# Kernel tuning notes

Hardware: AMD Instinct MI355X
Metric: run time of the kernel (lower is better)

## Reference

```python
import jax, jax.numpy as jnp
import numpy as np

B, A, H, V, L = 8192, 128, 256, 64, 20


def setup_inputs() -> dict:
    key = jax.random.key(0)
    ks = jax.random.split(key, 9)
    s = lambda k, sh: jax.random.normal(k, sh, dtype=jnp.float32) * 0.05
    return {
        "attrVector": jax.random.normal(ks[0], (B, A), dtype=jnp.float32),
        "W_a": s(ks[1], (H, A)), "b_a": s(ks[2], (H,)),
        "W_ih": s(ks[3], (4 * H, V)), "W_hh": s(ks[4], (4 * H, H)),
        "b_ih": s(ks[5], (4 * H,)), "b_hh": s(ks[6], (4 * H,)),
        "W_v": s(ks[7], (V, H)), "b_v": s(ks[8], (V,)),
    }


def _lstm_step(x, h, c, W_ih, W_hh, b_ih, b_hh):
    # PyTorch LSTM gate order: input, forget, cell(g), output
    gates = x @ W_ih.T + b_ih + h @ W_hh.T + b_hh  # [B, 4H]
    i, f, g, o = jnp.split(gates, 4, axis=-1)
    c_new = jax.nn.sigmoid(f) * c + jax.nn.sigmoid(i) * jnp.tanh(g)
    h_new = jax.nn.sigmoid(o) * jnp.tanh(c_new)
    return h_new, c_new


def reference(attrVector, W_a, b_a, W_ih, W_hh, b_ih, b_hh, W_v, b_v):
    batch = attrVector.shape[0]
    dt = attrVector.dtype
    # attr2hidden -> initial hidden state; cell state zeros (init_hidden)
    h = attrVector @ W_a.T + b_a                      # [B, H]
    c = jnp.zeros_like(h)
    # start-token step (all-zeros embedding)
    x0 = jnp.zeros((batch, V), dtype=dt)
    h, c = _lstm_step(x0, h, c, W_ih, W_hh, b_ih, b_hh)

    keys = jax.random.split(jax.random.key(42), L)

    def step(carry, k):
        h, c, slp, plp, ep = carry
        logits = h @ W_v.T + b_v                      # [B, V]
        logp = jax.nn.log_softmax(logits, axis=-1)
        plp = plp + jnp.sum(jnp.exp(logp) * logp, axis=-1)  # negative entropy
        ch = jax.random.categorical(k, logits, axis=-1)     # [B] int sample
        lp = jnp.take_along_axis(logp, ch[:, None], axis=-1)[:, 0]
        slp = slp + lp
        ep = ep * jnp.exp(lp)
        x = jax.nn.one_hot(ch, V, dtype=dt)
        h2, c2 = _lstm_step(x, h, c, W_ih, W_hh, b_ih, b_hh)
        return (h2, c2, slp, plp, ep), ch

    zeros = jnp.zeros((batch,), dtype=dt)
    ones = jnp.ones((batch,), dtype=dt)
    (_, _, slp, plp, ep), msgs = jax.lax.scan(step, (h, c, zeros, zeros, ones), keys)
    message = msgs.T.astype(jnp.int64) if msgs.dtype != jnp.int64 else msgs.T  # [B, L]
    return message, slp, plp, ep
```

## Files before the change

### kernel.cpp

```cpp
#include <hip/hip_runtime.h>
#include <stdint.h>

#define BATCH 8192
#define ADIM 128
#define HDIM 256
#define VDIM 64
#define NSTEP 20
#define TB 16
#define HSP 17
#define ASP 20

typedef union { float4 v; float f[4]; } F4;

__device__ __forceinline__ uint32_t rotl32(uint32_t x, uint32_t d) {
  return (x << d) | (x >> (32u - d));
}
__device__ __forceinline__ void tf4(uint32_t& x0, uint32_t& x1, int r0, int r1, int r2, int r3) {
  x0 += x1; x1 = rotl32(x1, r0); x1 ^= x0;
  x0 += x1; x1 = rotl32(x1, r1); x1 ^= x0;
  x0 += x1; x1 = rotl32(x1, r2); x1 ^= x0;
  x0 += x1; x1 = rotl32(x1, r3); x1 ^= x0;
}
__device__ __forceinline__ void threefry2x32(uint32_t k0, uint32_t k1, uint32_t x0, uint32_t x1,
                                             uint32_t& o0, uint32_t& o1) {
  uint32_t k2 = k0 ^ k1 ^ 0x1BD11BDAu;
  x0 += k0; x1 += k1;
  tf4(x0, x1, 13, 15, 26, 6);  x0 += k1; x1 += k2 + 1u;
  tf4(x0, x1, 17, 29, 16, 24); x0 += k2; x1 += k0 + 2u;
  tf4(x0, x1, 13, 15, 26, 6);  x0 += k0; x1 += k1 + 3u;
  tf4(x0, x1, 17, 29, 16, 24); x0 += k1; x1 += k2 + 4u;
  tf4(x0, x1, 13, 15, 26, 6);  x0 += k2; x1 += k0 + 5u;
  o0 = x0; o1 = x1;
}

__device__ __forceinline__ float sigm(float x) { return 1.0f / (1.0f + expf(-x)); }

__device__ __forceinline__ float bcast(float x, int t) {
  return __int_as_float(__builtin_amdgcn_readlane(__float_as_int(x), t));
}

__global__ void prep_kernel(const float* __restrict__ Whh, const float* __restrict__ Wv,
                            const float* __restrict__ Wa, const float* __restrict__ Wih,
                            float* __restrict__ ws) {
  int n = blockIdx.x * blockDim.x + threadIdx.x;
  int stride = gridDim.x * blockDim.x;
  float* WhhT4 = ws;
  float* WvT   = ws + 262144;
  float* WaT   = ws + 278528;
  float* WihT4 = ws + 311296;
  for (int i = n; i < 256 * 1024; i += stride) {
    int k = i >> 10, rem = i & 1023, u = rem >> 2, g = rem & 3;
    WhhT4[i] = Whh[((g << 8) + u) * 256 + k];
  }
  for (int i = n; i < 256 * 64; i += stride) { int k = i >> 6, v = i & 63; WvT[i] = Wv[v * 256 + k]; }
  for (int i = n; i < 128 * 256; i += stride) { int k = i >> 8, u = i & 255; WaT[i] = Wa[u * 128 + k]; }
  for (int i = n; i < 64 * 1024; i += stride) {
    int v = i >> 10, rem = i & 1023, u = rem >> 2, g = rem & 3;
    WihT4[i] = Wih[((g << 8) + u) * 64 + v];
  }
}

__global__ __launch_bounds__(256, 2) void sender_main(
    const float* __restrict__ attr, const float* __restrict__ b_a,
    const float* __restrict__ b_ih, const float* __restrict__ b_hh,
    const float* __restrict__ b_v,
    const float* __restrict__ WhhT4, const float* __restrict__ WvT,
    const float* __restrict__ WaT, const float* __restrict__ WihT4,
    float* __restrict__ out) {
  __shared__ float h_s[HDIM][HSP];
  __shared__ __align__(16) float attr_s[ADIM][ASP];
  __shared__ float slp_s[TB], plp_s[TB], ep_s[TB];
  __shared__ int ch_s[TB];

  const int tid = threadIdx.x;
  const int w = tid >> 6;
  const int lane = tid & 63;
  const int u = (w << 6) + lane;
  const int w4 = w << 2;
  const int b0 = blockIdx.x * TB;

  if (tid < TB) { slp_s[tid] = 0.0f; plp_s[tid] = 0.0f; ep_s[tid] = 1.0f; }

  {
    int r = tid >> 5;
    int cm = (tid & 31) << 2;
    #pragma unroll
    for (int pass = 0; pass < 2; ++pass) {
      int row = r + (pass << 3);
      F4 vv; vv.v = *(const float4*)&attr[(size_t)(b0 + row) * ADIM + cm];
      attr_s[cm + 0][row] = vv.f[0];
      attr_s[cm + 1][row] = vv.f[1];
      attr_s[cm + 2][row] = vv.f[2];
      attr_s[cm + 3][row] = vv.f[3];
    }
  }
  __syncthreads();

  {
    float acc[16];
    #pragma unroll
    for (int s = 0; s < 16; ++s) acc[s] = 0.0f;
    #pragma unroll 2
    for (int k = 0; k < ADIM; ++k) {
      F4 a0, a1, a2, a3;
      a0.v = *(const float4*)&attr_s[k][0];
      a1.v = *(const float4*)&attr_s[k][4];
      a2.v = *(const float4*)&attr_s[k][8];
      a3.v = *(const float4*)&attr_s[k][12];
      float wa = WaT[(k << 8) + u];
      #pragma unroll
      for (int j = 0; j < 4; ++j) {
        acc[j]      = fmaf(a0.f[j], wa, acc[j]);
        acc[4 + j]  = fmaf(a1.f[j], wa, acc[4 + j]);
        acc[8 + j]  = fmaf(a2.f[j], wa, acc[8 + j]);
        acc[12 + j] = fmaf(a3.f[j], wa, acc[12 + j]);
      }
    }
    float ba = b_a[u];
    #pragma unroll
    for (int s = 0; s < 16; ++s) h_s[u][s] = acc[s] + ba;
  }
  __syncthreads();

  float c_r[16];
  #pragma unroll
  for (int s = 0; s < 16; ++s) c_r[s] = 0.0f;

  float bg[4];
  #pragma unroll
  for (int g = 0; g < 4; ++g) bg[g] = b_ih[(g << 8) + u] + b_hh[(g << 8) + u];
  const float bv = b_v[lane];

  {
    float ga[16][4];
    #pragma unroll
    for (int s = 0; s < 16; ++s)
      #pragma unroll
      for (int g = 0; g < 4; ++g) ga[s][g] = 0.0f;
    #pragma unroll 1
    for (int kc = 0; kc < 16; ++kc) {
      const int k0 = kc << 4;
      const int kk = k0 + (lane & 15);
      float hch[16];
      #pragma unroll
      for (int s = 0; s < 16; ++s) hch[s] = h_s[kk][(s + w4) & 15];
      #pragma unroll
      for (int t = 0; t < 16; ++t) {
        const int k = k0 + t;
        F4 wv4; wv4.v = *(const float4*)&WhhT4[(k << 10) + (u << 2)];
        #pragma unroll
        for (int s = 0; s < 16; ++s) {
          float hb = bcast(hch[s], t);
          ga[s][0] = fmaf(hb, wv4.f[0], ga[s][0]);
          ga[s][1] = fmaf(hb, wv4.f[1], ga[s][1]);
          ga[s][2] = fmaf(hb, wv4.f[2], ga[s][2]);
          ga[s][3] = fmaf(hb, wv4.f[3], ga[s][3]);
        }
      }
    }
    __syncthreads();
    float hn[16];
    #pragma unroll
    for (int s = 0; s < 16; ++s) {
      float gi = ga[s][0] + bg[0];
      float gf = ga[s][1] + bg[1];
      float gg = ga[s][2] + bg[2];
      float go = ga[s][3] + bg[3];
      float cn = sigm(gf) * c_r[s] + sigm(gi) * tanhf(gg);
      hn[s] = sigm(go) * tanhf(cn);
      c_r[s] = cn;
    }
    #pragma unroll
    for (int s = 0; s < 16; ++s) h_s[u][(s + w4) & 15] = hn[s];
    __syncthreads();
  }

  #pragma unroll 1
  for (int l = 0; l < NSTEP; ++l) {
    uint32_t kl0, kl1;
    threefry2x32(0u, 42u, 0u, (uint32_t)l, kl0, kl1);

    const bool last = (l == NSTEP - 1);
    float la[4] = {0.0f, 0.0f, 0.0f, 0.0f};
    float ga[16][4];
    #pragma unroll
    for (int s = 0; s < 16; ++s)
      #pragma unroll
      for (int g = 0; g < 4; ++g) ga[s][g] = 0.0f;

    if (!last) {
      #pragma unroll 1
      for (int kc = 0; kc < 16; ++kc) {
        const int k0 = kc << 4;
        const int kk = k0 + (lane & 15);
        float hch[16];
        #pragma unroll
        for (int s = 0; s < 16; ++s) hch[s] = h_s[kk][(s + w4) & 15];
        #pragma unroll
        for (int t = 0; t < 16; ++t) {
          const int k = k0 + t;
          F4 wv4; wv4.v = *(const float4*)&WhhT4[(k << 10) + (u << 2)];
          float wvv = WvT[(k << 6) | lane];
          #pragma unroll
          for (int s = 0; s < 16; ++s) {
            float hb = bcast(hch[s], t);
            if (s < 4) la[s] = fmaf(hb, wvv, la[s]);
            ga[s][0] = fmaf(hb, wv4.f[0], ga[s][0]);
            ga[s][1] = fmaf(hb, wv4.f[1], ga[s][1]);
            ga[s][2] = fmaf(hb, wv4.f[2], ga[s][2]);
            ga[s][3] = fmaf(hb, wv4.f[3], ga[s][3]);
          }
        }
      }
    } else {
      #pragma unroll 1
      for (int kc = 0; kc < 16; ++kc) {
        const int k0 = kc << 4;
        const int kk = k0 + (lane & 15);
        float hch[4];
        #pragma unroll
        for (int s = 0; s < 4; ++s) hch[s] = h_s[kk][(s + w4) & 15];
        #pragma unroll
        for (int t = 0; t < 16; ++t) {
          const int k = k0 + t;
          float wvv = WvT[(k << 6) | lane];
          #pragma unroll
          for (int s = 0; s < 4; ++s) la[s] = fmaf(bcast(hch[s], t), wvv, la[s]);
        }
      }
    }

    #pragma unroll
    for (int db = 0; db < 4; ++db) {
      float x = la[db] + bv;
      float m = x;
      #pragma unroll
      for (int o = 32; o > 0; o >>= 1) m = fmaxf(m, __shfl_xor(m, o));
      float e = expf(x - m);
      float s = e;
      #pragma unroll
      for (int o = 32; o > 0; o >>= 1) s += __shfl_xor(s, o);
      float lse = logf(s);
      float logp = x - m - lse;
      float p = expf(logp);
      float pe = p * logp;
      #pragma unroll
      for (int o = 32; o > 0; o >>= 1) pe += __shfl_xor(pe, o);
      uint32_t idx = ((uint32_t)(b0 + w4 + db) << 6) | (uint32_t)lane;
      uint32_t r0, r1;
      threefry2x32(kl0, kl1, 0u, idx, r0, r1);
      uint32_t bits = r0 ^ r1;
      float f01 = __uint_as_float((bits >> 9) | 0x3f800000u) - 1.0f;
      const float TINY = 1.17549435e-38f;
      float uu2 = fmaxf(TINY, f01 + TINY);
      float gn = -logf(-logf(uu2));
      float y = gn + x;
      float by = y; int bi = lane;
      #pragma unroll
      for (int o = 32; o > 0; o >>= 1) {
        float oy = __shfl_xor(by, o);
        int oi = __shfl_xor(bi, o);
        if (oy > by || (oy == by && oi < bi)) { by = oy; bi = oi; }
      }
      float lp = __shfl(logp, bi, 64);
      if (lane == 0) {
        int bb = w4 + db;
        ch_s[bb] = bi;
        slp_s[bb] += lp;
        plp_s[bb] += pe;
        ep_s[bb] *= expf(lp);
        out[(size_t)(b0 + bb) * NSTEP + l] = (float)bi;
      }
    }

    if (!last) {
      __syncthreads();
      float hn[16];
      #pragma unroll
      for (int s = 0; s < 16; ++s) {
        const int sp = (s + w4) & 15;
        F4 wi; wi.v = *(const float4*)&WihT4[(ch_s[sp] << 10) + (u << 2)];
        float gi = ga[s][0] + wi.f[0] + bg[0];
        float gf = ga[s][1] + wi.f[1] + bg[1];
        float gg = ga[s][2] + wi.f[2] + bg[2];
        float go = ga[s][3] + wi.f[3] + bg[3];
        float cn = sigm(gf) * c_r[s] + sigm(gi) * tanhf(gg);
        hn[s] = sigm(go) * tanhf(cn);
        c_r[s] = cn;
      }
      #pragma unroll
      for (int s = 0; s < 16; ++s) h_s[u][(s + w4) & 15] = hn[s];
      __syncthreads();
    }
  }

  __syncthreads();
  if (tid < TB) {
    int bb = b0 + tid;
    out[(size_t)BATCH * NSTEP + bb]             = slp_s[tid];
    out[(size_t)BATCH * NSTEP + BATCH + bb]     = plp_s[tid];
    out[(size_t)BATCH * NSTEP + 2 * BATCH + bb] = ep_s[tid];
  }
}

extern "C" void kernel_launch(void* const* d_in, const int* in_sizes, int n_in,
                              void* d_out, int out_size, void* d_ws, size_t ws_size,
                              hipStream_t stream) {
  const float* attr = (const float*)d_in[0];
  const float* W_a  = (const float*)d_in[1];
  const float* b_a  = (const float*)d_in[2];
  const float* W_ih = (const float*)d_in[3];
  const float* W_hh = (const float*)d_in[4];
  const float* b_ih = (const float*)d_in[5];
  const float* b_hh = (const float*)d_in[6];
  const float* W_v  = (const float*)d_in[7];
  const float* b_v  = (const float*)d_in[8];
  float* ws = (float*)d_ws;

  prep_kernel<<<256, 256, 0, stream>>>(W_hh, W_v, W_a, W_ih, ws);
  sender_main<<<BATCH / TB, 256, 0, stream>>>(
      attr, b_a, b_ih, b_hh, b_v,
      ws, ws + 262144, ws + 278528, ws + 311296,
      (float*)d_out);
}
```

Baseline: 1.451 ms.

## Store hidden state batch-major and read it with broadcast float4 LDS loads

Changes the shared hidden-state layout from [H][17] to [TB][H]. Each wave now reads four consecutive hidden values per sample with a uniform-address float4 LDS load, replacing the per-k readlane broadcasts. The vocab projection reads W_v directly in its row layout with float4 loads, so the WvT transpose in the prep kernel is dropped. This cuts readlane instructions and scalar dependencies but moves more traffic onto LDS reads, and the hidden-state stores now have a different bank pattern.

```diff
diff --git a/kernel.cpp b/kernel.cpp
--- a/kernel.cpp
+++ b/kernel.cpp
@@ -7,7 +7,6 @@
 #define VDIM 64
 #define NSTEP 20
 #define TB 16
-#define HSP 17
 #define ASP 20
 
 typedef union { float4 v; float f[4]; } F4;
@@ -35,28 +34,21 @@
 
 __device__ __forceinline__ float sigm(float x) { return 1.0f / (1.0f + expf(-x)); }
 
-__device__ __forceinline__ float bcast(float x, int t) {
-  return __int_as_float(__builtin_amdgcn_readlane(__float_as_int(x), t));
-}
-
-__global__ void prep_kernel(const float* __restrict__ Whh, const float* __restrict__ Wv,
-                            const float* __restrict__ Wa, const float* __restrict__ Wih,
-                            float* __restrict__ ws) {
+__global__ void prep_kernel(const float* __restrict__ Whh, const float* __restrict__ Wa,
+                            const float* __restrict__ Wih, float* __restrict__ ws) {
   int n = blockIdx.x * blockDim.x + threadIdx.x;
   int stride = gridDim.x * blockDim.x;
   float* WhhT4 = ws;
-  float* WvT   = ws + 262144;
-  float* WaT   = ws + 278528;
-  float* WihT4 = ws + 311296;
+  float* WaT   = ws + 262144;
+  float* WihT4 = ws + 294912;
   for (int i = n; i < 256 * 1024; i += stride) {
     int k = i >> 10, rem = i & 1023, u = rem >> 2, g = rem & 3;
     WhhT4[i] = Whh[((g << 8) + u) * 256 + k];
   }
-  for (int i = n; i < 256 * 64; i += stride) { int k = i >> 6, v = i & 63; WvT[i] = Wv[v * 256 + k]; }
-  for (int i = n; i < 128 * 256; i += stride) { int k = i >> 8, u = i & 255; WaT[i] = Wa[u * 128 + k]; }
+  for (int i = n; i < 128 * 256; i += stride) { int k = i >> 8, uu = i & 255; WaT[i] = Wa[uu * 128 + k]; }
   for (int i = n; i < 64 * 1024; i += stride) {
-    int v = i >> 10, rem = i & 1023, u = rem >> 2, g = rem & 3;
-    WihT4[i] = Wih[((g << 8) + u) * 64 + v];
+    int v = i >> 10, rem = i & 1023, uu = rem >> 2, g = rem & 3;
+    WihT4[i] = Wih[((g << 8) + uu) * 64 + v];
   }
 }
 
@@ -64,10 +56,10 @@
     const float* __restrict__ attr, const float* __restrict__ b_a,
     const float* __restrict__ b_ih, const float* __restrict__ b_hh,
     const float* __restrict__ b_v,
-    const float* __restrict__ WhhT4, const float* __restrict__ WvT,
+    const float* __restrict__ WhhT4, const float* __restrict__ Wv2,
     const float* __restrict__ WaT, const float* __restrict__ WihT4,
     float* __restrict__ out) {
-  __shared__ float h_s[HDIM][HSP];
+  __shared__ __align__(16) float h_s[TB][HDIM];
   __shared__ __align__(16) float attr_s[ADIM][ASP];
   __shared__ float slp_s[TB], plp_s[TB], ep_s[TB];
   __shared__ int ch_s[TB];
@@ -76,8 +68,15 @@
   const int w = tid >> 6;
   const int lane = tid & 63;
   const int u = (w << 6) + lane;
+  const int uu4 = u << 2;
   const int w4 = w << 2;
   const int b0 = blockIdx.x * TB;
+
+  int hr[16];
+  #pragma unroll
+  for (int s = 0; s < 16; ++s) hr[s] = (s + w4) & 15;
+
+  const float* Wv2r = Wv2 + (lane << 8);
 
   if (tid < TB) { slp_s[tid] = 0.0f; plp_s[tid] = 0.0f; ep_s[tid] = 1.0f; }
 
@@ -118,7 +117,7 @@
     }
     float ba = b_a[u];
     #pragma unroll
-    for (int s = 0; s < 16; ++s) h_s[u][s] = acc[s] + ba;
+    for (int s = 0; s < 16; ++s) h_s[s][u] = acc[s] + ba;
   }
   __syncthreads();
 
@@ -139,22 +138,24 @@
       for (int g = 0; g < 4; ++g) ga[s][g] = 0.0f;
     #pragma unroll 1
     for (int kc = 0; kc < 16; ++kc) {
-      const int k0 = kc << 4;
-      const int kk = k0 + (lane & 15);
-      float hch[16];
-      #pragma unroll
-      for (int s = 0; s < 16; ++s) hch[s] = h_s[kk][(s + w4) & 15];
-      #pragma unroll
-      for (int t = 0; t < 16; ++t) {
-        const int k = k0 + t;
-        F4 wv4; wv4.v = *(const float4*)&WhhT4[(k << 10) + (u << 2)];
+      #pragma unroll
+      for (int kg = 0; kg < 4; ++kg) {
+        const int k0 = (kc << 4) + (kg << 2);
+        F4 wk[4];
+        #pragma unroll
+        for (int j = 0; j < 4; ++j)
+          wk[j].v = *(const float4*)&WhhT4[((k0 + j) << 10) + uu4];
         #pragma unroll
         for (int s = 0; s < 16; ++s) {
-          float hb = bcast(hch[s], t);
-          ga[s][0] = fmaf(hb, wv4.f[0], ga[s][0]);
-          ga[s][1] = fmaf(hb, wv4.f[1], ga[s][1]);
-          ga[s][2] = fmaf(hb, wv4.f[2], ga[s][2]);
-          ga[s][3] = fmaf(hb, wv4.f[3], ga[s][3]);
+          F4 h4; h4.v = *(const float4*)&h_s[hr[s]][k0];
+          #pragma unroll
+          for (int j = 0; j < 4; ++j) {
+            float hb = h4.f[j];
+            ga[s][0] = fmaf(hb, wk[j].f[0], ga[s][0]);
+            ga[s][1] = fmaf(hb, wk[j].f[1], ga[s][1]);
+            ga[s][2] = fmaf(hb, wk[j].f[2], ga[s][2]);
+            ga[s][3] = fmaf(hb, wk[j].f[3], ga[s][3]);
+          }
         }
       }
     }
@@ -171,7 +172,7 @@
       c_r[s] = cn;
     }
     #pragma unroll
-    for (int s = 0; s < 16; ++s) h_s[u][(s + w4) & 15] = hn[s];
+    for (int s = 0; s < 16; ++s) h_s[hr[s]][u] = hn[s];
     __syncthreads();
   }
 
@@ -191,41 +192,49 @@
     if (!last) {
       #pragma unroll 1
       for (int kc = 0; kc < 16; ++kc) {
-        const int k0 = kc << 4;
-        const int kk = k0 + (lane & 15);
-        float hch[16];
         #pragma unroll
-        for (int s = 0; s < 16; ++s) hch[s] = h_s[kk][(s + w4) & 15];
-        #pragma unroll
-        for (int t = 0; t < 16; ++t) {
-          const int k = k0 + t;
-          F4 wv4; wv4.v = *(const float4*)&WhhT4[(k << 10) + (u << 2)];
-          float wvv = WvT[(k << 6) | lane];
+        for (int kg = 0; kg < 4; ++kg) {
+          const int k0 = (kc << 4) + (kg << 2);
+          F4 wk[4], wvv;
+          #pragma unroll
+          for (int j = 0; j < 4; ++j)
+            wk[j].v = *(const float4*)&WhhT4[((k0 + j) << 10) + uu4];
+          wvv.v = *(const float4*)(Wv2r + k0);
           #pragma unroll
           for (int s = 0; s < 16; ++s) {
-            float hb = bcast(hch[s], t);
-            if (s < 4) la[s] = fmaf(hb, wvv, la[s]);
-            ga[s][0] = fmaf(hb, wv4.f[0], ga[s][0]);
-            ga[s][1] = fmaf(hb, wv4.f[1], ga[s][1]);
-            ga[s][2] = fmaf(hb, wv4.f[2], ga[s][2]);
-            ga[s][3] = fmaf(hb, wv4.f[3], ga[s][3]);
+            F4 h4; h4.v = *(const float4*)&h_s[hr[s]][k0];
+            if (s < 4) {
+              la[s] = fmaf(h4.f[0], wvv.f[0], la[s]);
+              la[s] = fmaf(h4.f[1], wvv.f[1], la[s]);
+              la[s] = fmaf(h4.f[2], wvv.f[2], la[s]);
+              la[s] = fmaf(h4.f[3], wvv.f[3], la[s]);
+            }
+            #pragma unroll
+            for (int j = 0; j < 4; ++j) {
+              float hb = h4.f[j];
+              ga[s][0] = fmaf(hb, wk[j].f[0], ga[s][0]);
+              ga[s][1] = fmaf(hb, wk[j].f[1], ga[s][1]);
+              ga[s][2] = fmaf(hb, wk[j].f[2], ga[s][2]);
+              ga[s][3] = fmaf(hb, wk[j].f[3], ga[s][3]);
+            }
           }
         }
       }
     } else {
       #pragma unroll 1
       for (int kc = 0; kc < 16; ++kc) {
-        const int k0 = kc << 4;
-        const int kk = k0 + (lane & 15);
-        float hch[4];
         #pragma unroll
-        for (int s = 0; s < 4; ++s) hch[s] = h_s[kk][(s + w4) & 15];
-        #pragma unroll
-        for (int t = 0; t < 16; ++t) {
-          const int k = k0 + t;
-          float wvv = WvT[(k << 6) | lane];
+        for (int kg = 0; kg < 4; ++kg) {
+          const int k0 = (kc << 4) + (kg << 2);
+          F4 wvv; wvv.v = *(const float4*)(Wv2r + k0);
           #pragma unroll
-          for (int s = 0; s < 4; ++s) la[s] = fmaf(bcast(hch[s], t), wvv, la[s]);
+          for (int s = 0; s < 4; ++s) {
+            F4 h4; h4.v = *(const float4*)&h_s[hr[s]][k0];
+            la[s] = fmaf(h4.f[0], wvv.f[0], la[s]);
+            la[s] = fmaf(h4.f[1], wvv.f[1], la[s]);
+            la[s] = fmaf(h4.f[2], wvv.f[2], la[s]);
+            la[s] = fmaf(h4.f[3], wvv.f[3], la[s]);
+          }
         }
       }
     }
@@ -278,8 +287,8 @@
       float hn[16];
       #pragma unroll
       for (int s = 0; s < 16; ++s) {
-        const int sp = (s + w4) & 15;
-        F4 wi; wi.v = *(const float4*)&WihT4[(ch_s[sp] << 10) + (u << 2)];
+        const int sp = hr[s];
+        F4 wi; wi.v = *(const float4*)&WihT4[(ch_s[sp] << 10) + uu4];
         float gi = ga[s][0] + wi.f[0] + bg[0];
         float gf = ga[s][1] + wi.f[1] + bg[1];
         float gg = ga[s][2] + wi.f[2] + bg[2];
@@ -289,7 +298,7 @@
         c_r[s] = cn;
       }
       #pragma unroll
-      for (int s = 0; s < 16; ++s) h_s[u][(s + w4) & 15] = hn[s];
+      for (int s = 0; s < 16; ++s) h_s[hr[s]][u] = hn[s];
       __syncthreads();
     }
   }
@@ -317,9 +326,9 @@
   const float* b_v  = (const float*)d_in[8];
   float* ws = (float*)d_ws;
 
-  prep_kernel<<<256, 256, 0, stream>>>(W_hh, W_v, W_a, W_ih, ws);
+  prep_kernel<<<256, 256, 0, stream>>>(W_hh, W_a, W_ih, ws);
   sender_main<<<BATCH / TB, 256, 0, stream>>>(
       attr, b_a, b_ih, b_hh, b_v,
-      ws, ws + 262144, ws + 278528, ws + 311296,
+      ws, W_v, ws + 262144, ws + 294912,
       (float*)d_out);
 }
```

After: 1.876 ms. 29.3% more time.

## Use packed FP32 FMA inline asm and move cell state to LDS

Applied to the files above, without the earlier changes.

Replaces the scalar FMA inner loop of the recurrent GEMV with hand-written inline asm. It reads two h values per lane pair into SGPRs and applies v_pk_fma_f32 over gate pairs, which halves the FMA instruction count. The cell state moves from registers into shared memory to free VGPRs for the 2-waves-per-SIMD launch bound. The cost is extra LDS traffic and fixed SGPR clobbers that can limit compiler scheduling. The h_s write also moves inside the same loop, without the earlier staging array.

```diff
diff --git a/kernel.cpp b/kernel.cpp
--- a/kernel.cpp
+++ b/kernel.cpp
@@ -10,7 +10,8 @@
 #define HSP 17
 #define ASP 20
 
-typedef union { float4 v; float f[4]; } F4;
+typedef float v2f __attribute__((ext_vector_type(2)));
+typedef union { float4 v; v2f h2[2]; float f[4]; } F4;
 
 __device__ __forceinline__ uint32_t rotl32(uint32_t x, uint32_t d) {
   return (x << d) | (x >> (32u - d));
@@ -53,12 +54,72 @@
     WhhT4[i] = Whh[((g << 8) + u) * 256 + k];
   }
   for (int i = n; i < 256 * 64; i += stride) { int k = i >> 6, v = i & 63; WvT[i] = Wv[v * 256 + k]; }
-  for (int i = n; i < 128 * 256; i += stride) { int k = i >> 8, u = i & 255; WaT[i] = Wa[u * 128 + k]; }
+  for (int i = n; i < 128 * 256; i += stride) { int k = i >> 8, uu = i & 255; WaT[i] = Wa[uu * 128 + k]; }
   for (int i = n; i < 64 * 1024; i += stride) {
-    int v = i >> 10, rem = i & 1023, u = rem >> 2, g = rem & 3;
-    WihT4[i] = Wih[((g << 8) + u) * 64 + v];
-  }
-}
+    int v = i >> 10, rem = i & 1023, uu = rem >> 2, g = rem & 3;
+    WihT4[i] = Wih[((g << 8) + uu) * 64 + v];
+  }
+}
+
+#define SPBLK(SA, SB, T0, T1)                                                              \
+  asm("v_readlane_b32 s90, %[ha], " #T0 "\n\t"                                             \
+      "v_readlane_b32 s91, %[ha], " #T1 "\n\t"                                             \
+      "v_readlane_b32 s92, %[hb], " #T0 "\n\t"                                             \
+      "v_readlane_b32 s93, %[hb], " #T1 "\n\t"                                             \
+      "v_pk_fma_f32 %[aA0], s[90:91], %[w0A], %[aA0] op_sel:[0,0,0] op_sel_hi:[0,1,1]\n\t" \
+      "v_pk_fma_f32 %[aA1], s[90:91], %[w1A], %[aA1] op_sel:[0,0,0] op_sel_hi:[0,1,1]\n\t" \
+      "v_pk_fma_f32 %[aA0], s[90:91], %[w0B], %[aA0] op_sel:[1,0,0] op_sel_hi:[1,1,1]\n\t" \
+      "v_pk_fma_f32 %[aA1], s[90:91], %[w1B], %[aA1] op_sel:[1,0,0] op_sel_hi:[1,1,1]\n\t" \
+      "v_pk_fma_f32 %[aB0], s[92:93], %[w0A], %[aB0] op_sel:[0,0,0] op_sel_hi:[0,1,1]\n\t" \
+      "v_pk_fma_f32 %[aB1], s[92:93], %[w1A], %[aB1] op_sel:[0,0,0] op_sel_hi:[0,1,1]\n\t" \
+      "v_pk_fma_f32 %[aB0], s[92:93], %[w0B], %[aB0] op_sel:[1,0,0] op_sel_hi:[1,1,1]\n\t" \
+      "v_pk_fma_f32 %[aB1], s[92:93], %[w1B], %[aB1] op_sel:[1,0,0] op_sel_hi:[1,1,1]"     \
+      : [aA0]"+v"(ga01[SA]), [aA1]"+v"(ga23[SA]),                                          \
+        [aB0]"+v"(ga01[SB]), [aB1]"+v"(ga23[SB])                                           \
+      : [ha]"v"(hch[SA]), [hb]"v"(hch[SB]),                                                \
+        [w0A]"v"(wkA.h2[0]), [w1A]"v"(wkA.h2[1]),                                          \
+        [w0B]"v"(wkB.h2[0]), [w1B]"v"(wkB.h2[1])                                           \
+      : "s90","s91","s92","s93")
+
+#define SPBLK_L(SA, SB, T0, T1)                                                            \
+  asm("v_readlane_b32 s90, %[ha], " #T0 "\n\t"                                             \
+      "v_readlane_b32 s91, %[ha], " #T1 "\n\t"                                             \
+      "v_readlane_b32 s92, %[hb], " #T0 "\n\t"                                             \
+      "v_readlane_b32 s93, %[hb], " #T1 "\n\t"                                             \
+      "v_pk_fma_f32 %[aA0], s[90:91], %[w0A], %[aA0] op_sel:[0,0,0] op_sel_hi:[0,1,1]\n\t" \
+      "v_pk_fma_f32 %[aA1], s[90:91], %[w1A], %[aA1] op_sel:[0,0,0] op_sel_hi:[0,1,1]\n\t" \
+      "v_pk_fma_f32 %[aA0], s[90:91], %[w0B], %[aA0] op_sel:[1,0,0] op_sel_hi:[1,1,1]\n\t" \
+      "v_pk_fma_f32 %[aA1], s[90:91], %[w1B], %[aA1] op_sel:[1,0,0] op_sel_hi:[1,1,1]\n\t" \
+      "v_fma_f32 %[lA], s90, %[wv0], %[lA]\n\t"                                            \
+      "v_fma_f32 %[lA], s91, %[wv1], %[lA]\n\t"                                            \
+      "v_pk_fma_f32 %[aB0], s[92:93], %[w0A], %[aB0] op_sel:[0,0,0] op_sel_hi:[0,1,1]\n\t" \
+      "v_pk_fma_f32 %[aB1], s[92:93], %[w1A], %[aB1] op_sel:[0,0,0] op_sel_hi:[0,1,1]\n\t" \
+      "v_pk_fma_f32 %[aB0], s[92:93], %[w0B], %[aB0] op_sel:[1,0,0] op_sel_hi:[1,1,1]\n\t" \
+      "v_pk_fma_f32 %[aB1], s[92:93], %[w1B], %[aB1] op_sel:[1,0,0] op_sel_hi:[1,1,1]\n\t" \
+      "v_fma_f32 %[lB], s92, %[wv0], %[lB]\n\t"                                            \
+      "v_fma_f32 %[lB], s93, %[wv1], %[lB]"                                                \
+      : [aA0]"+v"(ga01[SA]), [aA1]"+v"(ga23[SA]),                                          \
+        [aB0]"+v"(ga01[SB]), [aB1]"+v"(ga23[SB]),                                          \
+        [lA]"+v"(la[SA]), [lB]"+v"(la[SB])                                                 \
+      : [ha]"v"(hch[SA]), [hb]"v"(hch[SB]),                                                \
+        [w0A]"v"(wkA.h2[0]), [w1A]"v"(wkA.h2[1]),                                          \
+        [w0B]"v"(wkB.h2[0]), [w1B]"v"(wkB.h2[1]),                                          \
+        [wv0]"v"(wv0), [wv1]"v"(wv1)                                                       \
+      : "s90","s91","s92","s93")
+
+#define TPAIR(T0, T1)                                                  \
+  do {                                                                 \
+    F4 wkA, wkB;                                                       \
+    wkA.v = *(const float4*)&WhhT4[((k0 + T0) << 10) + uu4];           \
+    wkB.v = *(const float4*)&WhhT4[((k0 + T1) << 10) + uu4];           \
+    float wv0 = WvT[((k0 + T0) << 6) | lane];                          \
+    float wv1 = WvT[((k0 + T1) << 6) | lane];                          \
+    SPBLK_L(0, 1, T0, T1);                                             \
+    SPBLK_L(2, 3, T0, T1);                                             \
+    SPBLK(4, 5, T0, T1);   SPBLK(6, 7, T0, T1);                        \
+    SPBLK(8, 9, T0, T1);   SPBLK(10, 11, T0, T1);                      \
+    SPBLK(12, 13, T0, T1); SPBLK(14, 15, T0, T1);                      \
+  } while (0)
 
 __global__ __launch_bounds__(256, 2) void sender_main(
     const float* __restrict__ attr, const float* __restrict__ b_a,
@@ -68,6 +129,7 @@
     const float* __restrict__ WaT, const float* __restrict__ WihT4,
     float* __restrict__ out) {
   __shared__ float h_s[HDIM][HSP];
+  __shared__ float c_s[HDIM][HSP];
   __shared__ __align__(16) float attr_s[ADIM][ASP];
   __shared__ float slp_s[TB], plp_s[TB], ep_s[TB];
   __shared__ int ch_s[TB];
@@ -76,6 +138,7 @@
   const int w = tid >> 6;
   const int lane = tid & 63;
   const int u = (w << 6) + lane;
+  const int uu4 = u << 2;
   const int w4 = w << 2;
   const int b0 = blockIdx.x * TB;
 
@@ -122,10 +185,6 @@
   }
   __syncthreads();
 
-  float c_r[16];
-  #pragma unroll
-  for (int s = 0; s < 16; ++s) c_r[s] = 0.0f;
-
   float bg[4];
   #pragma unroll
   for (int g = 0; g < 4; ++g) bg[g] = b_ih[(g << 8) + u] + b_hh[(g << 8) + u];
@@ -147,7 +206,7 @@
       #pragma unroll
       for (int t = 0; t < 16; ++t) {
         const int k = k0 + t;
-        F4 wv4; wv4.v = *(const float4*)&WhhT4[(k << 10) + (u << 2)];
+        F4 wv4; wv4.v = *(const float4*)&WhhT4[(k << 10) + uu4];
         #pragma unroll
         for (int s = 0; s < 16; ++s) {
           float hb = bcast(hch[s], t);
@@ -159,19 +218,17 @@
       }
     }
     __syncthreads();
-    float hn[16];
     #pragma unroll
     for (int s = 0; s < 16; ++s) {
+      const int sp = (s + w4) & 15;
       float gi = ga[s][0] + bg[0];
       float gf = ga[s][1] + bg[1];
       float gg = ga[s][2] + bg[2];
       float go = ga[s][3] + bg[3];
-      float cn = sigm(gf) * c_r[s] + sigm(gi) * tanhf(gg);
-      hn[s] = sigm(go) * tanhf(cn);
-      c_r[s] = cn;
-    }
-    #pragma unroll
-    for (int s = 0; s < 16; ++s) h_s[u][(s + w4) & 15] = hn[s];
+      float cn = sigm(gf) * 0.0f + sigm(gi) * tanhf(gg);
+      c_s[u][sp] = cn;
+      h_s[u][sp] = sigm(go) * tanhf(cn);
+    }
     __syncthreads();
   }
 
@@ -182,13 +239,11 @@
 
     const bool last = (l == NSTEP - 1);
     float la[4] = {0.0f, 0.0f, 0.0f, 0.0f};
-    float ga[16][4];
-    #pragma unroll
-    for (int s = 0; s < 16; ++s)
-      #pragma unroll
-      for (int g = 0; g < 4; ++g) ga[s][g] = 0.0f;
+    v2f ga01[16], ga23[16];
 
     if (!last) {
+      #pragma unroll
+      for (int s = 0; s < 16; ++s) { ga01[s] = (v2f)(0.0f); ga23[s] = (v2f)(0.0f); }
       #pragma unroll 1
       for (int kc = 0; kc < 16; ++kc) {
         const int k0 = kc << 4;
@@ -196,21 +251,8 @@
         float hch[16];
         #pragma unroll
         for (int s = 0; s < 16; ++s) hch[s] = h_s[kk][(s + w4) & 15];
-        #pragma unroll
-        for (int t = 0; t < 16; ++t) {
-          const int k = k0 + t;
-          F4 wv4; wv4.v = *(const float4*)&WhhT4[(k << 10) + (u << 2)];
-          float wvv = WvT[(k << 6) | lane];
-          #pragma unroll
-          for (int s = 0; s < 16; ++s) {
-            float hb = bcast(hch[s], t);
-            if (s < 4) la[s] = fmaf(hb, wvv, la[s]);
-            ga[s][0] = fmaf(hb, wv4.f[0], ga[s][0]);
-            ga[s][1] = fmaf(hb, wv4.f[1], ga[s][1]);
-            ga[s][2] = fmaf(hb, wv4.f[2], ga[s][2]);
-            ga[s][3] = fmaf(hb, wv4.f[3], ga[s][3]);
-          }
-        }
+        TPAIR(0, 1);   TPAIR(2, 3);   TPAIR(4, 5);   TPAIR(6, 7);
+        TPAIR(8, 9);   TPAIR(10, 11); TPAIR(12, 13); TPAIR(14, 15);
       }
     } else {
       #pragma unroll 1
@@ -275,21 +317,19 @@
 
     if (!last) {
       __syncthreads();
-      float hn[16];
       #pragma unroll
       for (int s = 0; s < 16; ++s) {
         const int sp = (s + w4) & 15;
-        F4 wi; wi.v = *(const float4*)&WihT4[(ch_s[sp] << 10) + (u << 2)];
-        float gi = ga[s][0] + wi.f[0] + bg[0];
-        float gf = ga[s][1] + wi.f[1] + bg[1];
-        float gg = ga[s][2] + wi.f[2] + bg[2];
-        float go = ga[s][3] + wi.f[3] + bg[3];
-        float cn = sigm(gf) * c_r[s] + sigm(gi) * tanhf(gg);
-        hn[s] = sigm(go) * tanhf(cn);
-        c_r[s] = cn;
-      }
-      #pragma unroll
-      for (int s = 0; s < 16; ++s) h_s[u][(s + w4) & 15] = hn[s];
+        F4 wi; wi.v = *(const float4*)&WihT4[(ch_s[sp] << 10) + uu4];
+        float cr = c_s[u][sp];
+        float gi = ga01[s].x + wi.f[0] + bg[0];
+        float gf = ga01[s].y + wi.f[1] + bg[1];
+        float gg = ga23[s].x + wi.f[2] + bg[2];
+        float go = ga23[s].y + wi.f[3] + bg[3];
+        float cn = sigm(gf) * cr + sigm(gi) * tanhf(gg);
+        c_s[u][sp] = cn;
+        h_s[u][sp] = sigm(go) * tanhf(cn);
+      }
       __syncthreads();
     }
   }
```

New measurement: 1.618 ms. 1.12x slower.

## Retile LSTM recurrence so each wave covers 128 units over 8 samples

Applied to the files above, without the earlier changes.

In the main loop, each wave now computes gates for two 64-unit groups over 8 samples instead of one 64-unit group over 16 samples. This halves the cross-lane readlane broadcasts of h per FMA, in exchange for twice as many W_hh weight loads per FMA. Cell state moves from registers into an LDS array to free VGPRs. The W_v transpose is re-laid out so each thread does one float4 load every four k steps instead of a scalar load per step.

```diff
diff --git a/kernel.cpp b/kernel.cpp
--- a/kernel.cpp
+++ b/kernel.cpp
@@ -45,18 +45,21 @@
   int n = blockIdx.x * blockDim.x + threadIdx.x;
   int stride = gridDim.x * blockDim.x;
   float* WhhT4 = ws;
-  float* WvT   = ws + 262144;
+  float* WvT4  = ws + 262144;
   float* WaT   = ws + 278528;
   float* WihT4 = ws + 311296;
   for (int i = n; i < 256 * 1024; i += stride) {
     int k = i >> 10, rem = i & 1023, u = rem >> 2, g = rem & 3;
     WhhT4[i] = Whh[((g << 8) + u) * 256 + k];
   }
-  for (int i = n; i < 256 * 64; i += stride) { int k = i >> 6, v = i & 63; WvT[i] = Wv[v * 256 + k]; }
-  for (int i = n; i < 128 * 256; i += stride) { int k = i >> 8, u = i & 255; WaT[i] = Wa[u * 128 + k]; }
+  for (int i = n; i < 64 * 64 * 4; i += stride) {
+    int kg = i >> 8, v = (i >> 2) & 63, j = i & 3;
+    WvT4[i] = Wv[v * 256 + (kg << 2) + j];
+  }
+  for (int i = n; i < 128 * 256; i += stride) { int k = i >> 8, uu = i & 255; WaT[i] = Wa[uu * 128 + k]; }
   for (int i = n; i < 64 * 1024; i += stride) {
-    int v = i >> 10, rem = i & 1023, u = rem >> 2, g = rem & 3;
-    WihT4[i] = Wih[((g << 8) + u) * 64 + v];
+    int v = i >> 10, rem = i & 1023, uu = rem >> 2, g = rem & 3;
+    WihT4[i] = Wih[((g << 8) + uu) * 64 + v];
   }
 }
 
@@ -64,10 +67,11 @@
     const float* __restrict__ attr, const float* __restrict__ b_a,
     const float* __restrict__ b_ih, const float* __restrict__ b_hh,
     const float* __restrict__ b_v,
-    const float* __restrict__ WhhT4, const float* __restrict__ WvT,
+    const float* __restrict__ WhhT4, const float* __restrict__ WvT4,
     const float* __restrict__ WaT, const float* __restrict__ WihT4,
     float* __restrict__ out) {
   __shared__ float h_s[HDIM][HSP];
+  __shared__ float c_s[HDIM][HSP];
   __shared__ __align__(16) float attr_s[ADIM][ASP];
   __shared__ float slp_s[TB], plp_s[TB], ep_s[TB];
   __shared__ int ch_s[TB];
@@ -77,6 +81,11 @@
   const int lane = tid & 63;
   const int u = (w << 6) + lane;
   const int w4 = w << 2;
+  const int ug = (w & 1) << 7;
+  const int u0 = ug + lane;
+  const int u1 = ug + 64 + lane;
+  const int sg = (w >> 1) << 3;
+  const int rot = (w & 1) << 2;
   const int b0 = blockIdx.x * TB;
 
   if (tid < TB) { slp_s[tid] = 0.0f; plp_s[tid] = 0.0f; ep_s[tid] = 1.0f; }
@@ -122,16 +131,12 @@
   }
   __syncthreads();
 
-  float c_r[16];
-  #pragma unroll
-  for (int s = 0; s < 16; ++s) c_r[s] = 0.0f;
-
-  float bg[4];
-  #pragma unroll
-  for (int g = 0; g < 4; ++g) bg[g] = b_ih[(g << 8) + u] + b_hh[(g << 8) + u];
   const float bv = b_v[lane];
 
   {
+    float bgi[4];
+    #pragma unroll
+    for (int g = 0; g < 4; ++g) bgi[g] = b_ih[(g << 8) + u] + b_hh[(g << 8) + u];
     float ga[16][4];
     #pragma unroll
     for (int s = 0; s < 16; ++s)
@@ -159,20 +164,25 @@
       }
     }
     __syncthreads();
-    float hn[16];
     #pragma unroll
     for (int s = 0; s < 16; ++s) {
-      float gi = ga[s][0] + bg[0];
-      float gf = ga[s][1] + bg[1];
-      float gg = ga[s][2] + bg[2];
-      float go = ga[s][3] + bg[3];
-      float cn = sigm(gf) * c_r[s] + sigm(gi) * tanhf(gg);
-      hn[s] = sigm(go) * tanhf(cn);
-      c_r[s] = cn;
-    }
-    #pragma unroll
-    for (int s = 0; s < 16; ++s) h_s[u][(s + w4) & 15] = hn[s];
+      const int sp = (s + w4) & 15;
+      float gi = ga[s][0] + bgi[0];
+      float gf = ga[s][1] + bgi[1];
+      float gg = ga[s][2] + bgi[2];
+      float go = ga[s][3] + bgi[3];
+      float cn = sigm(gf) * 0.0f + sigm(gi) * tanhf(gg);
+      c_s[u][sp] = cn;
+      h_s[u][sp] = sigm(go) * tanhf(cn);
+    }
     __syncthreads();
+  }
+
+  float bg0[4], bg1[4];
+  #pragma unroll
+  for (int g = 0; g < 4; ++g) {
+    bg0[g] = b_ih[(g << 8) + u0] + b_hh[(g << 8) + u0];
+    bg1[g] = b_ih[(g << 8) + u1] + b_hh[(g << 8) + u1];
   }
 
   #pragma unroll 1
@@ -182,33 +192,40 @@
 
     const bool last = (l == NSTEP - 1);
     float la[4] = {0.0f, 0.0f, 0.0f, 0.0f};
-    float ga[16][4];
-    #pragma unroll
-    for (int s = 0; s < 16; ++s)
-      #pragma unroll
-      for (int g = 0; g < 4; ++g) ga[s][g] = 0.0f;
+    float ga0[8][4], ga1[8][4];
+    #pragma unroll
+    for (int s = 0; s < 8; ++s)
+      #pragma unroll
+      for (int g = 0; g < 4; ++g) { ga0[s][g] = 0.0f; ga1[s][g] = 0.0f; }
 
     if (!last) {
       #pragma unroll 1
       for (int kc = 0; kc < 16; ++kc) {
         const int k0 = kc << 4;
         const int kk = k0 + (lane & 15);
-        float hch[16];
-        #pragma unroll
-        for (int s = 0; s < 16; ++s) hch[s] = h_s[kk][(s + w4) & 15];
+        float hch[8];
+        #pragma unroll
+        for (int s = 0; s < 8; ++s) hch[s] = h_s[kk][sg + ((s + rot) & 7)];
+        F4 wvv;
         #pragma unroll
         for (int t = 0; t < 16; ++t) {
           const int k = k0 + t;
-          F4 wv4; wv4.v = *(const float4*)&WhhT4[(k << 10) + (u << 2)];
-          float wvv = WvT[(k << 6) | lane];
+          F4 wk0, wk1;
+          wk0.v = *(const float4*)&WhhT4[(k << 10) + (u0 << 2)];
+          wk1.v = *(const float4*)&WhhT4[(k << 10) + (u1 << 2)];
+          if ((t & 3) == 0) wvv.v = *(const float4*)&WvT4[((k >> 2) << 8) + (lane << 2)];
           #pragma unroll
-          for (int s = 0; s < 16; ++s) {
+          for (int s = 0; s < 8; ++s) {
             float hb = bcast(hch[s], t);
-            if (s < 4) la[s] = fmaf(hb, wvv, la[s]);
-            ga[s][0] = fmaf(hb, wv4.f[0], ga[s][0]);
-            ga[s][1] = fmaf(hb, wv4.f[1], ga[s][1]);
-            ga[s][2] = fmaf(hb, wv4.f[2], ga[s][2]);
-            ga[s][3] = fmaf(hb, wv4.f[3], ga[s][3]);
+            if (s < 4) la[s] = fmaf(hb, wvv.f[t & 3], la[s]);
+            ga0[s][0] = fmaf(hb, wk0.f[0], ga0[s][0]);
+            ga0[s][1] = fmaf(hb, wk0.f[1], ga0[s][1]);
+            ga0[s][2] = fmaf(hb, wk0.f[2], ga0[s][2]);
+            ga0[s][3] = fmaf(hb, wk0.f[3], ga0[s][3]);
+            ga1[s][0] = fmaf(hb, wk1.f[0], ga1[s][0]);
+            ga1[s][1] = fmaf(hb, wk1.f[1], ga1[s][1]);
+            ga1[s][2] = fmaf(hb, wk1.f[2], ga1[s][2]);
+            ga1[s][3] = fmaf(hb, wk1.f[3], ga1[s][3]);
           }
         }
       }
@@ -219,13 +236,14 @@
         const int kk = k0 + (lane & 15);
         float hch[4];
         #pragma unroll
-        for (int s = 0; s < 4; ++s) hch[s] = h_s[kk][(s + w4) & 15];
+        for (int s = 0; s < 4; ++s) hch[s] = h_s[kk][sg + ((s + rot) & 7)];
+        F4 wvv;
         #pragma unroll
         for (int t = 0; t < 16; ++t) {
           const int k = k0 + t;
-          float wvv = WvT[(k << 6) | lane];
+          if ((t & 3) == 0) wvv.v = *(const float4*)&WvT4[((k >> 2) << 8) + (lane << 2)];
           #pragma unroll
-          for (int s = 0; s < 4; ++s) la[s] = fmaf(bcast(hch[s], t), wvv, la[s]);
+          for (int s = 0; s < 4; ++s) la[s] = fmaf(bcast(hch[s], t), wvv.f[t & 3], la[s]);
         }
       }
     }
@@ -275,21 +293,34 @@
 
     if (!last) {
       __syncthreads();
-      float hn[16];
-      #pragma unroll
-      for (int s = 0; s < 16; ++s) {
-        const int sp = (s + w4) & 15;
-        F4 wi; wi.v = *(const float4*)&WihT4[(ch_s[sp] << 10) + (u << 2)];
-        float gi = ga[s][0] + wi.f[0] + bg[0];
-        float gf = ga[s][1] + wi.f[1] + bg[1];
-        float gg = ga[s][2] + wi.f[2] + bg[2];
-        float go = ga[s][3] + wi.f[3] + bg[3];
-        float cn = sigm(gf) * c_r[s] + sigm(gi) * tanhf(gg);
-        hn[s] = sigm(go) * tanhf(cn);
-        c_r[s] = cn;
-      }
-      #pragma unroll
-      for (int s = 0; s < 16; ++s) h_s[u][(s + w4) & 15] = hn[s];
+      #pragma unroll
+      for (int s = 0; s < 8; ++s) {
+        const int sp = sg + ((s + rot) & 7);
+        const int ch = ch_s[sp];
+        F4 wi0, wi1;
+        wi0.v = *(const float4*)&WihT4[(ch << 10) + (u0 << 2)];
+        wi1.v = *(const float4*)&WihT4[(ch << 10) + (u1 << 2)];
+        {
+          float cr = c_s[u0][sp];
+          float gi = ga0[s][0] + wi0.f[0] + bg0[0];
+          float gf = ga0[s][1] + wi0.f[1] + bg0[1];
+          float gg = ga0[s][2] + wi0.f[2] + bg0[2];
+          float go = ga0[s][3] + wi0.f[3] + bg0[3];
+          float cn = sigm(gf) * cr + sigm(gi) * tanhf(gg);
+          c_s[u0][sp] = cn;
+          h_s[u0][sp] = sigm(go) * tanhf(cn);
+        }
+        {
+          float cr = c_s[u1][sp];
+          float gi = ga1[s][0] + wi1.f[0] + bg1[0];
+          float gf = ga1[s][1] + wi1.f[1] + bg1[1];
+          float gg = ga1[s][2] + wi1.f[2] + bg1[2];
+          float go = ga1[s][3] + wi1.f[3] + bg1[3];
+          float cn = sigm(gf) * cr + sigm(gi) * tanhf(gg);
+          c_s[u1][sp] = cn;
+          h_s[u1][sp] = sigm(go) * tanhf(cn);
+        }
+      }
       __syncthreads();
     }
   }
```

New measurement: 2.217 ms. 52.8% more time.
